# Kernel optimization log

Hardware: AMD Instinct MI355X
Metric: run time of the kernel (lower is better)

Reference implementation:

```python
import jax, jax.numpy as jnp
import numpy as np

DIM = 384
RED = 16
PAIR = 128
EPS = 1e-5


def setup_inputs() -> dict:
    key = jax.random.key(0)
    ks = jax.random.split(key, 6)
    b, m = 2, 512
    x = jax.random.normal(ks[0], (b, m, DIM), dtype=jnp.float32)
    ln_gamma = jnp.ones((DIM,), dtype=jnp.float32)
    ln_beta = jnp.zeros((DIM,), dtype=jnp.float32)
    w_red = jax.random.normal(ks[1], (DIM, RED), dtype=jnp.float32) / np.sqrt(DIM)
    b_red = jax.random.normal(ks[2], (RED,), dtype=jnp.float32) * 0.02
    w_out = jax.random.normal(ks[3], (RED * RED, PAIR), dtype=jnp.float32) / np.sqrt(RED * RED)
    b_out = jax.random.normal(ks[4], (PAIR,), dtype=jnp.float32) * 0.02
    return {"x": x, "ln_gamma": ln_gamma, "ln_beta": ln_beta,
            "w_red": w_red, "b_red": b_red, "w_out": w_out, "b_out": b_out}


def reference(x, ln_gamma, ln_beta, w_red, b_red, w_out, b_out):
    # LayerNorm over last dim (eps=1e-5, torch default)
    mu = jnp.mean(x, axis=-1, keepdims=True)
    var = jnp.mean(jnp.square(x - mu), axis=-1, keepdims=True)
    xn = (x - mu) * jax.lax.rsqrt(var + EPS) * ln_gamma + ln_beta
    # Linear dim -> 16
    xr = jnp.einsum('bmd,dr->bmr', xn, w_red) + b_red  # (b, m, 16)
    # Full pairwise outer product + projection: same math as
    # einsum('bmi,bnj->bmnij') -> reshape (i j) -> Linear(256, pair_dim),
    # fused so the (i,j) axes contract directly with w_out reshaped to (16,16,pair).
    wr = w_out.reshape(RED, RED, PAIR)
    out = jnp.einsum('bmi,bnj,ijp->bmnp', xr, xr, wr) + b_out  # (b, m, m, pair)
    return out
```

## Files before the change

### kernel.cpp

```cpp
#include <hip/hip_runtime.h>
#include <hip/hip_bf16.h>

#define DIM 384
#define RED 16
#define PAIR 128
#define B 2
#define M 512
#define EPSV 1e-5f

typedef float f32x4 __attribute__((ext_vector_type(4)));

__global__ __launch_bounds__(128) void opm_k1(
    const float* __restrict__ x, const float* __restrict__ g,
    const float* __restrict__ be, const float* __restrict__ w_red,
    const float* __restrict__ b_red, const float* __restrict__ w_out,
    float* __restrict__ xr_out, float* __restrict__ T_out) {
  const int row = blockIdx.x;
  const int tid = threadIdx.x;
  const float* xrow = x + (size_t)row * DIM;

  __shared__ float xn[DIM];
  __shared__ float xr_s[RED];
  __shared__ float rs[2][2];
  __shared__ float psum[8][RED];

  float v0 = xrow[tid];
  float v1 = xrow[tid + 128];
  float v2 = xrow[tid + 256];
  float s  = v0 + v1 + v2;
  float sq = v0 * v0 + v1 * v1 + v2 * v2;
  #pragma unroll
  for (int off = 32; off > 0; off >>= 1) {
    s  += __shfl_down(s, off);
    sq += __shfl_down(sq, off);
  }
  if ((tid & 63) == 0) { rs[0][tid >> 6] = s; rs[1][tid >> 6] = sq; }
  __syncthreads();
  const float mean = (rs[0][0] + rs[0][1]) * (1.0f / DIM);
  const float var  = (rs[1][0] + rs[1][1]) * (1.0f / DIM) - mean * mean;
  const float rstd = rsqrtf(var + EPSV);

  xn[tid]       = (v0 - mean) * rstd * g[tid]       + be[tid];
  xn[tid + 128] = (v1 - mean) * rstd * g[tid + 128] + be[tid + 128];
  xn[tid + 256] = (v2 - mean) * rstd * g[tid + 256] + be[tid + 256];
  __syncthreads();

  {
    const int r = tid & 15;
    const int part = tid >> 4;
    float ps = 0.0f;
    const int d0 = part * 48;
    #pragma unroll 8
    for (int d = d0; d < d0 + 48; ++d) ps += xn[d] * w_red[d * RED + r];
    psum[part][r] = ps;
  }
  __syncthreads();
  if (tid < RED) {
    float v = b_red[tid];
    #pragma unroll
    for (int q = 0; q < 8; ++q) v += psum[q][tid];
    xr_s[tid] = v;
    xr_out[(size_t)row * RED + tid] = v;
  }
  __syncthreads();

  {
    const int p = tid;
    const float* W = w_out + p;
    float* Trow = T_out + (size_t)row * RED * PAIR + p;
    #pragma unroll
    for (int i = 0; i < RED; ++i) {
      float acc = 0.0f;
      #pragma unroll
      for (int j = 0; j < RED; ++j) acc += xr_s[j] * W[(i * RED + j) * PAIR];
      Trow[i * PAIR] = acc;
    }
  }
}

__global__ __launch_bounds__(256) void opm_k2(
    const float* __restrict__ xr, const float* __restrict__ T,
    const float* __restrict__ b_out, float* __restrict__ out) {
  const int nc  = blockIdx.x & 63;
  const int mt  = (blockIdx.x >> 6) & 7;
  const int b   = blockIdx.x >> 9;
  const int tid = threadIdx.x;
  const int p4  = (tid & 31) * 4;
  const int n   = nc * 8 + (tid >> 5);

  __shared__ float a_s[64 * RED];

  {
    const float* src = xr + (size_t)(b * M + mt * 64) * RED;
    #pragma unroll
    for (int k = 0; k < 4; ++k) a_s[tid + k * 256] = src[tid + k * 256];
  }

  const f32x4 bias = *reinterpret_cast<const f32x4*>(&b_out[p4]);

  f32x4 t[RED];
  const float* Tb = T + ((size_t)(b * M + n) * RED) * PAIR + p4;
  #pragma unroll
  for (int i = 0; i < RED; ++i)
    t[i] = *reinterpret_cast<const f32x4*>(&Tb[i * PAIR]);
  __syncthreads();

  float* outp = out + (((size_t)(b * M + mt * 64) * M + n) * PAIR) + p4;
  #pragma unroll 4
  for (int m = 0; m < 64; ++m) {
    const f32x4 a0 = *reinterpret_cast<const f32x4*>(&a_s[m * RED + 0]);
    const f32x4 a1 = *reinterpret_cast<const f32x4*>(&a_s[m * RED + 4]);
    const f32x4 a2 = *reinterpret_cast<const f32x4*>(&a_s[m * RED + 8]);
    const f32x4 a3 = *reinterpret_cast<const f32x4*>(&a_s[m * RED + 12]);
    f32x4 acc = bias;
    acc += a0.x * t[0];
    acc += a0.y * t[1];
    acc += a0.z * t[2];
    acc += a0.w * t[3];
    acc += a1.x * t[4];
    acc += a1.y * t[5];
    acc += a1.z * t[6];
    acc += a1.w * t[7];
    acc += a2.x * t[8];
    acc += a2.y * t[9];
    acc += a2.z * t[10];
    acc += a2.w * t[11];
    acc += a3.x * t[12];
    acc += a3.y * t[13];
    acc += a3.z * t[14];
    acc += a3.w * t[15];
    __builtin_nontemporal_store(acc, reinterpret_cast<f32x4*>(outp));
    outp += (size_t)M * PAIR;
  }
}

extern "C" void kernel_launch(void* const* d_in, const int* in_sizes, int n_in,
                              void* d_out, int out_size, void* d_ws, size_t ws_size,
                              hipStream_t stream) {
  const float* x       = (const float*)d_in[0];
  const float* ln_g    = (const float*)d_in[1];
  const float* ln_b    = (const float*)d_in[2];
  const float* w_red   = (const float*)d_in[3];
  const float* b_red   = (const float*)d_in[4];
  const float* w_out   = (const float*)d_in[5];
  const float* b_out   = (const float*)d_in[6];
  float* out = (float*)d_out;

  float* xr = (float*)d_ws;
  float* T  = xr + (size_t)B * M * RED;

  opm_k1<<<B * M, 128, 0, stream>>>(x, ln_g, ln_b, w_red, b_red, w_out, xr, T);
  opm_k2<<<B * (M / 64) * (M / 8), 256, 0, stream>>>(xr, T, b_out, out);
}
```

Before: 71.07 us.

## Use bf16 MFMA for pairwise projection and store intermediates in bf16

The first kernel now writes xr and the per-row T matrix as bf16, with T transposed so each output column's 16 coefficients are contiguous. The second kernel replaces the fp32 vector FMA loop with 16x16x32 bf16 MFMA instructions: half the K dimension is zero-padded, and the results are scattered as scalar stores. This is meant to cut ALU work and intermediate memory traffic. In exchange it gives up the vectorised nontemporal output stores and reduces precision to bf16 inputs.

Measured after the change: 57.32 us. 1.24x faster.

```diff
diff --git a/kernel.cpp b/kernel.cpp
--- a/kernel.cpp
+++ b/kernel.cpp
@@ -9,12 +9,19 @@
 #define EPSV 1e-5f
 
 typedef float f32x4 __attribute__((ext_vector_type(4)));
+typedef short bf16x8 __attribute__((ext_vector_type(8)));
+
+__device__ __forceinline__ unsigned short f2bf(float f) {
+  union { float f; unsigned u; } v; v.f = f;
+  unsigned r = v.u + 0x7fffu + ((v.u >> 16) & 1u);
+  return (unsigned short)(r >> 16);
+}
 
 __global__ __launch_bounds__(128) void opm_k1(
     const float* __restrict__ x, const float* __restrict__ g,
     const float* __restrict__ be, const float* __restrict__ w_red,
     const float* __restrict__ b_red, const float* __restrict__ w_out,
-    float* __restrict__ xr_out, float* __restrict__ T_out) {
+    unsigned short* __restrict__ xr_bf, unsigned short* __restrict__ T_bf) {
   const int row = blockIdx.x;
   const int tid = threadIdx.x;
   const float* xrow = x + (size_t)row * DIM;
@@ -60,77 +67,76 @@
     #pragma unroll
     for (int q = 0; q < 8; ++q) v += psum[q][tid];
     xr_s[tid] = v;
-    xr_out[(size_t)row * RED + tid] = v;
+    xr_bf[(size_t)row * RED + tid] = f2bf(v);
   }
   __syncthreads();
 
   {
     const int p = tid;
     const float* W = w_out + p;
-    float* Trow = T_out + (size_t)row * RED * PAIR + p;
+    float acc[RED];
     #pragma unroll
     for (int i = 0; i < RED; ++i) {
-      float acc = 0.0f;
+      float a = 0.0f;
       #pragma unroll
-      for (int j = 0; j < RED; ++j) acc += xr_s[j] * W[(i * RED + j) * PAIR];
-      Trow[i * PAIR] = acc;
+      for (int j = 0; j < RED; ++j) a += xr_s[j] * W[(i * RED + j) * PAIR];
+      acc[i] = a;
     }
+    unsigned int w0[4], w1[4];
+    #pragma unroll
+    for (int k = 0; k < 4; ++k) {
+      w0[k] = (unsigned)f2bf(acc[2*k])     | ((unsigned)f2bf(acc[2*k+1]) << 16);
+      w1[k] = (unsigned)f2bf(acc[8+2*k])   | ((unsigned)f2bf(acc[8+2*k+1]) << 16);
+    }
+    unsigned int* dst = (unsigned int*)(T_bf + ((size_t)row * PAIR + p) * RED);
+    #pragma unroll
+    for (int k = 0; k < 4; ++k) { dst[k] = w0[k]; dst[4+k] = w1[k]; }
   }
 }
 
 __global__ __launch_bounds__(256) void opm_k2(
-    const float* __restrict__ xr, const float* __restrict__ T,
+    const unsigned short* __restrict__ xr_bf, const unsigned short* __restrict__ T_bf,
     const float* __restrict__ b_out, float* __restrict__ out) {
-  const int nc  = blockIdx.x & 63;
-  const int mt  = (blockIdx.x >> 6) & 7;
-  const int b   = blockIdx.x >> 9;
-  const int tid = threadIdx.x;
-  const int p4  = (tid & 31) * 4;
-  const int n   = nc * 8 + (tid >> 5);
+  const int nb = blockIdx.x & 127;
+  const int mt = (blockIdx.x >> 7) & 7;
+  const int b  = blockIdx.x >> 10;
+  const int wave = threadIdx.x >> 6;
+  const int lane = threadIdx.x & 63;
+  const int q = lane >> 4;
+  const int r = lane & 15;
+  const int n = nb * 4 + wave;
 
-  __shared__ float a_s[64 * RED];
+  bf16x8 bv[8];
+  const unsigned short* Tb = T_bf + ((size_t)(b * M + n) * PAIR) * RED;
+  #pragma unroll
+  for (int pb = 0; pb < 8; ++pb) {
+    bf16x8 v = {0, 0, 0, 0, 0, 0, 0, 0};
+    if (q < 2) v = *(const bf16x8*)(Tb + (pb * 16 + r) * RED + q * 8);
+    bv[pb] = v;
+  }
+  float bias[8];
+  #pragma unroll
+  for (int pb = 0; pb < 8; ++pb) bias[pb] = b_out[pb * 16 + r];
 
-  {
-    const float* src = xr + (size_t)(b * M + mt * 64) * RED;
+  const size_t MROW = (size_t)M * PAIR;
+
+  #pragma unroll
+  for (int ms = 0; ms < 4; ++ms) {
+    const int m0 = mt * 64 + ms * 16;
+    bf16x8 av = {0, 0, 0, 0, 0, 0, 0, 0};
+    if (q < 2) av = *(const bf16x8*)(xr_bf + (size_t)(b * M + m0 + r) * RED + q * 8);
+
+    float* outbase = out + ((size_t)(b * M + m0 + q * 4) * M + n) * PAIR + r;
     #pragma unroll
-    for (int k = 0; k < 4; ++k) a_s[tid + k * 256] = src[tid + k * 256];
-  }
-
-  const f32x4 bias = *reinterpret_cast<const f32x4*>(&b_out[p4]);
-
-  f32x4 t[RED];
-  const float* Tb = T + ((size_t)(b * M + n) * RED) * PAIR + p4;
-  #pragma unroll
-  for (int i = 0; i < RED; ++i)
-    t[i] = *reinterpret_cast<const f32x4*>(&Tb[i * PAIR]);
-  __syncthreads();
-
-  float* outp = out + (((size_t)(b * M + mt * 64) * M + n) * PAIR) + p4;
-  #pragma unroll 4
-  for (int m = 0; m < 64; ++m) {
-    const f32x4 a0 = *reinterpret_cast<const f32x4*>(&a_s[m * RED + 0]);
-    const f32x4 a1 = *reinterpret_cast<const f32x4*>(&a_s[m * RED + 4]);
-    const f32x4 a2 = *reinterpret_cast<const f32x4*>(&a_s[m * RED + 8]);
-    const f32x4 a3 = *reinterpret_cast<const f32x4*>(&a_s[m * RED + 12]);
-    f32x4 acc = bias;
-    acc += a0.x * t[0];
-    acc += a0.y * t[1];
-    acc += a0.z * t[2];
-    acc += a0.w * t[3];
-    acc += a1.x * t[4];
-    acc += a1.y * t[5];
-    acc += a1.z * t[6];
-    acc += a1.w * t[7];
-    acc += a2.x * t[8];
-    acc += a2.y * t[9];
-    acc += a2.z * t[10];
-    acc += a2.w * t[11];
-    acc += a3.x * t[12];
-    acc += a3.y * t[13];
-    acc += a3.z * t[14];
-    acc += a3.w * t[15];
-    __builtin_nontemporal_store(acc, reinterpret_cast<f32x4*>(outp));
-    outp += (size_t)M * PAIR;
+    for (int pb = 0; pb < 8; ++pb) {
+      f32x4 acc = {bias[pb], bias[pb], bias[pb], bias[pb]};
+      acc = __builtin_amdgcn_mfma_f32_16x16x32_bf16(av, bv[pb], acc, 0, 0, 0);
+      float* o = outbase + pb * 16;
+      o[0]        = acc[0];
+      o[MROW]     = acc[1];
+      o[2 * MROW] = acc[2];
+      o[3 * MROW] = acc[3];
+    }
   }
 }
 
@@ -146,9 +152,9 @@
   const float* b_out   = (const float*)d_in[6];
   float* out = (float*)d_out;
 
-  float* xr = (float*)d_ws;
-  float* T  = xr + (size_t)B * M * RED;
+  unsigned short* xr_bf = (unsigned short*)d_ws;
+  unsigned short* T_bf  = xr_bf + (size_t)B * M * RED;
 
-  opm_k1<<<B * M, 128, 0, stream>>>(x, ln_g, ln_b, w_red, b_red, w_out, xr, T);
-  opm_k2<<<B * (M / 64) * (M / 8), 256, 0, stream>>>(xr, T, b_out, out);
+  opm_k1<<<B * M, 128, 0, stream>>>(x, ln_g, ln_b, w_red, b_red, w_out, xr_bf, T_bf);
+  opm_k2<<<B * (M / 64) * (M / 4), 256, 0, stream>>>(xr_bf, T_bf, b_out, out);
 }
```
